# Optimization experiments

Measured on AMD Instinct MI355X. Metric: run time of the kernel, lower is better.

The kernel has to match this reference:

```python
import jax, jax.numpy as jnp
import numpy as np

FEAT_STRIDE = 16
NEG_OV, POS_OV = 0.3, 0.7
RPN_BATCH = 256
NUM_FG = int(0.5 * RPN_BATCH)  # RPN_FG_FRACTION * RPN_BATCHSIZE


def _gen_anchors(base=16, ratios=(0.5, 1.0, 2.0), scales=(4, 8, 16)):
    # 3D extension of the classic generate_anchors: ratio warps w/h, scale multiplies all dims
    ctr = (base - 1) / 2.0
    rows = []
    for r in ratios:
        for s in scales:
            w = base * s * np.sqrt(1.0 / r)
            h = base * s * np.sqrt(r)
            d = float(base * s)
            rows.append([ctr - 0.5 * (w - 1), ctr - 0.5 * (h - 1),
                         ctr + 0.5 * (w - 1), ctr + 0.5 * (h - 1),
                         ctr - 0.5 * (d - 1), ctr + 0.5 * (d - 1)])
    return np.asarray(rows, np.float32)


def setup_inputs() -> dict:
    key = jax.random.key(0)
    ks = jax.random.split(key, 8)
    B, H, W, D, K, A = 2, 48, 48, 24, 20, 9
    cls = jax.random.normal(ks[0], (B, 2 * A, H, W, D), jnp.float32)
    x1 = jax.random.uniform(ks[1], (B, K)) * 600.0
    y1 = jax.random.uniform(ks[2], (B, K)) * 600.0
    z1 = jax.random.uniform(ks[3], (B, K)) * 300.0
    whd = 16.0 + jax.random.uniform(ks[4], (B, K, 3)) * jnp.array([104.0, 104.0, 48.0])
    x2 = jnp.minimum(x1 + whd[..., 0], 767.0)
    y2 = jnp.minimum(y1 + whd[..., 1], 767.0)
    z2 = jnp.minimum(z1 + whd[..., 2], 383.0)
    cid = jax.random.randint(ks[5], (B, K), 1, 4).astype(jnp.float32)
    gt_boxes = jnp.stack([x1, y1, x2, y2, z1, z2, cid], axis=2)
    im_info = jnp.tile(jnp.array([[768.0, 768.0, 384.0]], jnp.float32), (B, 1))
    total = H * W * D * A
    return {
        'rpn_cls_score': cls,
        'gt_boxes': gt_boxes,
        'im_info': im_info,
        'num_boxes': jnp.full((B,), K, jnp.int32),
        'anchors': jnp.asarray(_gen_anchors()),
        'rand_fg': jax.random.uniform(ks[6], (B, total)),
        'rand_bg': jax.random.uniform(ks[7], (B, total)),
    }


def _overlaps(anc, gt):
    # anc: (N,6) [x1,y1,x2,y2,z1,z2]; gt: (B,K,7) -> IoU (B,N,K)
    aw = anc[:, 2] - anc[:, 0] + 1.0
    ah = anc[:, 3] - anc[:, 1] + 1.0
    ad = anc[:, 5] - anc[:, 4] + 1.0
    a_area = aw * ah * ad  # (N,)
    gw = gt[:, :, 2] - gt[:, :, 0] + 1.0
    gh = gt[:, :, 3] - gt[:, :, 1] + 1.0
    gd = gt[:, :, 5] - gt[:, :, 4] + 1.0
    g_area = gw * gh * gd  # (B,K)
    iw = jnp.clip(jnp.minimum(anc[None, :, None, 2], gt[:, None, :, 2]) -
                  jnp.maximum(anc[None, :, None, 0], gt[:, None, :, 0]) + 1.0, 0.0)
    ih = jnp.clip(jnp.minimum(anc[None, :, None, 3], gt[:, None, :, 3]) -
                  jnp.maximum(anc[None, :, None, 1], gt[:, None, :, 1]) + 1.0, 0.0)
    idp = jnp.clip(jnp.minimum(anc[None, :, None, 5], gt[:, None, :, 5]) -
                   jnp.maximum(anc[None, :, None, 4], gt[:, None, :, 4]) + 1.0, 0.0)
    inter = iw * ih * idp
    ov = inter / (a_area[None, :, None] + g_area[:, None, :] - inter)
    gt_zero = (gw == 1.0) & (gh == 1.0) & (gd == 1.0)
    a_zero = (aw == 1.0) & (ah == 1.0) & (ad == 1.0)
    ov = jnp.where(gt_zero[:, None, :], 0.0, ov)
    ov = jnp.where(a_zero[None, :, None], -1.0, ov)
    return ov


def _transform(ex, gt):
    # ex: (N,6); gt: (B,N,6) -> (B,N,6) targets (dx,dy,dz,dw,dh,dd)
    ew = ex[:, 2] - ex[:, 0] + 1.0
    eh = ex[:, 3] - ex[:, 1] + 1.0
    ed = ex[:, 5] - ex[:, 4] + 1.0
    ecx = ex[:, 0] + 0.5 * (ew - 1.0)
    ecy = ex[:, 1] + 0.5 * (eh - 1.0)
    ecz = ex[:, 4] + 0.5 * (ed - 1.0)
    gw = gt[:, :, 2] - gt[:, :, 0] + 1.0
    gh = gt[:, :, 3] - gt[:, :, 1] + 1.0
    gd = gt[:, :, 5] - gt[:, :, 4] + 1.0
    gcx = gt[:, :, 0] + 0.5 * (gw - 1.0)
    gcy = gt[:, :, 1] + 0.5 * (gh - 1.0)
    gcz = gt[:, :, 4] + 0.5 * (gd - 1.0)
    return jnp.stack([(gcx - ecx[None]) / ew[None],
                      (gcy - ecy[None]) / eh[None],
                      (gcz - ecz[None]) / ed[None],
                      jnp.log(gw / ew[None]),
                      jnp.log(gh / eh[None]),
                      jnp.log(gd / ed[None])], axis=2)


def _rank(p):
    # rank of each element when sorted by descending priority, per row
    return jnp.argsort(jnp.argsort(-p, axis=1), axis=1)


def reference(rpn_cls_score, gt_boxes, im_info, num_boxes, anchors, rand_fg, rand_bg):
    B = gt_boxes.shape[0]
    H, W, D = rpn_cls_score.shape[2], rpn_cls_score.shape[3], rpn_cls_score.shape[4]
    A = anchors.shape[0]
    sx = jnp.arange(W, dtype=jnp.float32) * FEAT_STRIDE
    sy = jnp.arange(H, dtype=jnp.float32) * FEAT_STRIDE
    sz = jnp.arange(D, dtype=jnp.float32) * FEAT_STRIDE
    mx, my, mz = jnp.meshgrid(sx, sy, sz, indexing='xy')  # (H,W,D) each
    shifts = jnp.stack([mx.ravel(), my.ravel(), mx.ravel(), my.ravel(), mz.ravel(), mz.ravel()], axis=1)
    all_anchors = (anchors[None, :, :] + shifts[:, None, :]).reshape(-1, 6)  # (total,6)
    total = all_anchors.shape[0]
    inside = ((all_anchors[:, 0] >= 0) & (all_anchors[:, 1] >= 0) & (all_anchors[:, 4] >= 0) &
              (all_anchors[:, 2] < im_info[0, 1]) & (all_anchors[:, 3] < im_info[0, 0]) &
              (all_anchors[:, 5] < im_info[0, 2]))  # (total,)

    ov = _overlaps(all_anchors, gt_boxes)                       # (B,total,K)
    ov_m = jnp.where(inside[None, :, None], ov, -1.0)           # mask outside anchors
    max_ov = ov_m.max(axis=2)
    argmax_ov = jnp.argmax(ov_m, axis=2)                        # (B,total)

    labels = jnp.full((B, total), -1.0, jnp.float32)
    ins = inside[None, :]
    labels = jnp.where(ins & (max_ov < NEG_OV), 0.0, labels)
    gt_max = ov_m.max(axis=1)                                   # (B,K)
    gt_max = jnp.where(gt_max == 0.0, 1e-5, gt_max)
    tie = jnp.sum(ov_m == gt_max[:, None, :], axis=2) > 0
    labels = jnp.where(ins & tie, 1.0, labels)
    labels = jnp.where(ins & (max_ov >= POS_OV), 1.0, labels)

    # fg subsampling: randomly keep at most NUM_FG positives per image
    fg = labels == 1.0
    rk = _rank(jnp.where(fg, rand_fg, -1.0))
    labels = jnp.where(fg & (rk >= NUM_FG), -1.0, labels)
    # bg subsampling: keep RPN_BATCH - num_fg negatives per image
    num_bg = RPN_BATCH - jnp.sum(labels == 1.0, axis=1)         # (B,)
    bg = labels == 0.0
    rkb = _rank(jnp.where(bg, rand_bg, -1.0))
    labels = jnp.where(bg & (rkb >= num_bg[:, None]), -1.0, labels)

    assigned = jnp.take_along_axis(gt_boxes, argmax_ov[:, :, None], axis=1)  # (B,total,7)
    bbox_targets = _transform(all_anchors, assigned[:, :, :6])
    bbox_targets = jnp.where(inside[None, :, None], bbox_targets, 0.0)

    in_w = jnp.where(labels == 1.0, 1.0, 0.0)                   # RPN_BBOX_INSIDE_WEIGHTS[0]=1
    # replicate original bug: weights from the LAST image's example count
    num_examples = jnp.sum(labels[-1] >= 0.0).astype(jnp.float32)
    w = 1.0 / num_examples
    out_w = jnp.where(labels == 1.0, w, jnp.where(labels == 0.0, w, 0.0))

    labels_o = labels.reshape(B, H, W, D, A).transpose(0, 4, 1, 2, 3).reshape(B, 1, A * H * D, W)
    bt_o = bbox_targets.reshape(B, H, W, D, A * 6).transpose(0, 4, 1, 2, 3)
    iw_o = jnp.broadcast_to(in_w[:, :, None], (B, total, 6)).reshape(B, H, W, D, 6 * A).transpose(0, 4, 1, 2, 3)
    ow_o = jnp.broadcast_to(out_w[:, :, None], (B, total, 6)).reshape(B, H, W, D, 6 * A).transpose(0, 4, 1, 2, 3)
    return labels_o, bt_o, iw_o, ow_o
```

## Files before the change

### kernel.cpp

```cpp
#include <hip/hip_runtime.h>
#include <math.h>

#define BB 2
#define HH 48
#define WW 48
#define DD 24
#define KK 20
#define AA 9
#define TOTAL (HH*WW*DD*AA)
#define SPAT (HH*WW*DD)
#define OUT0N (BB*TOTAL)
#define CH 54
#define NB 4096
#define CAPB 256
#define FG_QUOTA 128
#define RPN_B 256
#define STRIDE_F 16.0f

#define O_REC    0
#define O_GTMAX  (OUT0N)
#define O_HIST   (O_GTMAX + BB*KK)
#define O_CUT    (O_HIST + 4*NB)
#define O_W      (O_CUT + 16)
#define O_LIST   (O_W + 1)

__device__ __forceinline__ unsigned enc_f(float f){
  unsigned u = __float_as_uint(f);
  return (u & 0x80000000u) ? ~u : (u | 0x80000000u);
}
__device__ __forceinline__ float dec_f(unsigned u){
  return (u & 0x80000000u) ? __uint_as_float(u & 0x7FFFFFFFu) : __uint_as_float(~u);
}
#define ENC_NEG1 0x407FFFFFu

__device__ __forceinline__ float iou_pre(float ax1,float ay1,float ax2,float ay2,
                                         float az1,float az2,float a_area,
                                         const float* g){
  #pragma clang fp contract(off)
  float iw = fminf(ax2,g[2]) - fmaxf(ax1,g[0]) + 1.0f; iw = fmaxf(iw,0.0f);
  float ih = fminf(ay2,g[3]) - fmaxf(ay1,g[1]) + 1.0f; ih = fmaxf(ih,0.0f);
  float id = fminf(az2,g[5]) - fmaxf(az1,g[4]) + 1.0f; id = fmaxf(id,0.0f);
  float inter = iw*ih*id;
  return inter / ((a_area + g[6]) - inter);
}

__device__ __forceinline__ void gt_derive(const float* gt7, float* g8){
  #pragma clang fp contract(off)
  float gw = gt7[2]-gt7[0]+1.0f, gh = gt7[3]-gt7[1]+1.0f, gd = gt7[5]-gt7[4]+1.0f;
  g8[0]=gt7[0]; g8[1]=gt7[1]; g8[2]=gt7[2]; g8[3]=gt7[3];
  g8[4]=gt7[4]; g8[5]=gt7[5]; g8[6]=gw*gh*gd; g8[7]=0.0f;
}

#define GM_SB 27
__global__ void __launch_bounds__(256) k_gtmax(const float* __restrict__ gt,
    const float* __restrict__ anc, const float* __restrict__ imi,
    unsigned* __restrict__ ws){
  __shared__ float s_gd[KK*8];
  __shared__ float s_a6[6];
  __shared__ float s_im[3];
  __shared__ unsigned s_max[KK];
  int tid = threadIdx.x;
  int a = blockIdx.y;
  int b = blockIdx.z;
  if (b == 0 && a == 0 && blockIdx.x < 16){
    int base = blockIdx.x*256 + tid;
    #pragma unroll
    for (int j=0;j<4;j++) ws[O_HIST + j*NB + base] = 0u;
  }
  if (tid < KK) gt_derive(&gt[(b*KK+tid)*7], &s_gd[tid*8]);
  if (tid < 6)  s_a6[tid] = anc[a*6+tid];
  if (tid < 3)  s_im[tid] = imi[tid];
  if (tid < KK) s_max[tid] = ENC_NEG1;
  __syncthreads();
  float rmax[KK];
  #pragma unroll
  for (int k=0;k<KK;k++) rmax[k] = -1.0f;
  int s0 = blockIdx.x*256 + tid;
  for (int j=0; j<8; j++){
    int s = s0 + j*(GM_SB*256);
    int d = s % DD; int s2 = s / DD;
    int w = s2 % WW; int h = s2 / WW;
    float fx = w*STRIDE_F, fy = h*STRIDE_F, fz = d*STRIDE_F;
    float ax1=s_a6[0]+fx, ay1=s_a6[1]+fy, ax2=s_a6[2]+fx;
    float ay2=s_a6[3]+fy, az1=s_a6[4]+fz, az2=s_a6[5]+fz;
    bool inside = (ax1>=0.f)&&(ay1>=0.f)&&(az1>=0.f)&&
                  (ax2<s_im[1])&&(ay2<s_im[0])&&(az2<s_im[2]);
    if (inside){
      #pragma clang fp contract(off)
      float aw = ax2-ax1+1.0f, ah = ay2-ay1+1.0f, ad = az2-az1+1.0f;
      float a_area = aw*ah*ad;
      #pragma unroll
      for (int k=0;k<KK;k++)
        rmax[k] = fmaxf(rmax[k], iou_pre(ax1,ay1,ax2,ay2,az1,az2,a_area,&s_gd[k*8]));
    }
  }
  #pragma unroll
  for (int k=0;k<KK;k++){
    float v = rmax[k];
    for (int off=32; off>0; off>>=1) v = fmaxf(v, __shfl_down(v, off, 64));
    if ((tid & 63) == 0) atomicMax(&s_max[k], enc_f(v));
  }
  __syncthreads();
  if (tid < KK) atomicMax(&ws[O_GTMAX + b*KK + tid], s_max[tid]);
}

__global__ void __launch_bounds__(256) k_label(const float* __restrict__ gt,
    const float* __restrict__ anc, const float* __restrict__ imi,
    const float* __restrict__ rfg, const float* __restrict__ rbg,
    unsigned* __restrict__ ws){
  __shared__ float s_gd[BB*KK*8];
  __shared__ float s_anc[AA*6];
  __shared__ float s_im[3];
  __shared__ float s_gm[BB*KK];
  int tid = threadIdx.x;
  if (tid < BB*KK) gt_derive(&gt[tid*7], &s_gd[tid*8]);
  for (int j=tid; j<AA*6; j+=256) s_anc[j] = anc[j];
  if (tid<3) s_im[tid] = imi[tid];
  if (tid<BB*KK){ float g = dec_f(ws[O_GTMAX+tid]); if (g==0.0f) g = 1e-5f; s_gm[tid]=g; }
  __syncthreads();
  int t = blockIdx.x*256 + tid;
  int d = t % DD; int r1 = t/DD;
  int w = r1 % WW; int r2 = r1/WW;
  int h = r2 % HH; int r3 = r2/HH;
  int a = r3 % AA; int b = r3/AA;
  int i = ((h*WW+w)*DD + d)*AA + a;
  float fx=w*STRIDE_F, fy=h*STRIDE_F, fz=d*STRIDE_F;
  float ax1=s_anc[a*6+0]+fx, ay1=s_anc[a*6+1]+fy, ax2=s_anc[a*6+2]+fx;
  float ay2=s_anc[a*6+3]+fy, az1=s_anc[a*6+4]+fz, az2=s_anc[a*6+5]+fz;
  bool inside = (ax1>=0.f)&&(ay1>=0.f)&&(az1>=0.f)&&
                (ax2<s_im[1])&&(ay2<s_im[0])&&(az2<s_im[2]);
  float L = -1.0f;
  int am = 0;
  if (inside){
    #pragma clang fp contract(off)
    float aw = ax2-ax1+1.0f, ah = ay2-ay1+1.0f, ad = az2-az1+1.0f;
    float a_area = aw*ah*ad;
    float mv = -2.0f; bool tie = false;
    #pragma unroll
    for (int k=0;k<KK;k++){
      float ov = iou_pre(ax1,ay1,ax2,ay2,az1,az2,a_area,&s_gd[(b*KK+k)*8]);
      if (ov > mv){ mv = ov; am = k; }
      tie = tie || (ov == s_gm[b*KK+k]);
    }
    if (mv < 0.3f) L = 0.0f;
    if (tie)       L = 1.0f;
    if (mv >= 0.7f) L = 1.0f;
  }
  unsigned code = (L==1.0f) ? 2u : ((L==0.0f) ? 1u : 0u);
  unsigned bucket = 0;
  if (code){
    int fl = (code==1u ? 2 : 0) + b;
    const float* ra = (code==1u) ? rbg : rfg;
    float r = ra[b*TOTAL + i];
    bucket = (unsigned)min(NB-1, (int)(r*(float)NB));
    unsigned pos = atomicAdd(&ws[O_HIST + fl*NB + bucket], 1u);
    if (pos < CAPB) ((int*)ws)[O_LIST + ((fl*NB + (int)bucket)<<8) + pos] = i;
  }
  ws[O_REC + t] = code | ((unsigned)am<<2) | (bucket<<7);
}

__global__ void __launch_bounds__(256) k_cuts(unsigned* __restrict__ ws){
  int fl = blockIdx.x; int tid = threadIdx.x;
  int b = fl & 1; int isbg = fl >> 1;
  const int CHK = NB/256;
  __shared__ unsigned ps[256];
  __shared__ unsigned s_fg;
  if (tid == 0) s_fg = 0u;
  __syncthreads();
  unsigned part = 0;
  int hi = NB - CHK*tid;
  for (int j = hi-CHK; j < hi; j++) part += ws[O_HIST + fl*NB + j];
  if (isbg){
    unsigned pf = 0;
    for (int j = tid*CHK; j < (tid+1)*CHK; j++) pf += ws[O_HIST + b*NB + j];
    atomicAdd(&s_fg, pf);
  }
  ps[tid] = part;
  __syncthreads();
  for (int off=1; off<256; off<<=1){
    unsigned v = (tid>=off) ? ps[tid-off] : 0u;
    __syncthreads();
    ps[tid] += v;
    __syncthreads();
  }
  unsigned N = ps[255];
  unsigned excl = ps[tid] - part;
  unsigned F = isbg ? s_fg : N;
  int quota = isbg ? (RPN_B - (int)min(F, (unsigned)FG_QUOTA)) : FG_QUOTA;
  if (fl == 3 && tid == 0){
    int fgk = min((int)F, FG_QUOTA);
    int bgk = min((int)N, RPN_B - fgk);
    ((float*)ws)[O_W] = 1.0f / (float)(fgk + bgk);
  }
  int* cut = (int*)&ws[O_CUT + fl*4];
  if ((int)N <= quota){
    if (tid==0){ cut[0] = -1; cut[1] = 0; cut[2] = quota; cut[3] = 0; }
    return;
  }
  unsigned cum = excl;
  for (int bk = hi-1; bk >= hi-CHK; bk--){
    unsigned c = ws[O_HIST + fl*NB + bk];
    if (c > 0u && (unsigned)(quota-1) >= cum && (unsigned)(quota-1) < cum + c){
      cut[0] = bk; cut[1] = (int)cum; cut[2] = quota; cut[3] = (int)c;
    }
    cum += c;
  }
}

__global__ void __launch_bounds__(256) k_out(const float* __restrict__ gt,
    const float* __restrict__ anc, const float* __restrict__ imi,
    const float* __restrict__ rfg, const float* __restrict__ rbg,
    float* __restrict__ out, const unsigned* __restrict__ ws){
  __shared__ float s_gt[BB*KK*7];
  __shared__ float s_anc[AA*6];
  __shared__ float s_im[3];
  __shared__ float s_w;
  int tid = threadIdx.x;
  for (int j=tid; j<BB*KK*7; j+=256) s_gt[j] = gt[j];
  for (int j=tid; j<AA*6; j+=256) s_anc[j] = anc[j];
  if (tid<3) s_im[tid] = imi[tid];
  if (tid==0) s_w = ((const float*)ws)[O_W];
  __syncthreads();
  int t = blockIdx.x*256 + tid;
  int d = t % DD; int r1=t/DD; int w=r1%WW; int r2=r1/WW;
  int h = r2 % HH; int r3=r2/HH; int a=r3%AA; int b=r3/AA;
  unsigned rec = ws[O_REC + t];
  unsigned code = rec & 3u;
  int am = (int)((rec>>2) & 31u);
  int bucket = (int)((rec>>7) & 4095u);
  float L = (code==2u) ? 1.0f : ((code==1u) ? 0.0f : -1.0f);
  if (code){
    int isbg = (code==1u);
    int fl = isbg*2 + b;
    const int* cut = (const int*)&ws[O_CUT + fl*4];
    int cutb = cut[0];
    if (cutb >= 0){
      if (bucket < cutb) L = -1.0f;
      else if (bucket == cutb){
        int rank_base = cut[1], quota = cut[2];
        int n = min(cut[3], CAPB);
        int i = ((h*WW+w)*DD + d)*AA + a;
        const float* ra = isbg ? rbg : rfg;
        float ri = ra[b*TOTAL + i];
        const int* lst = (const int*)ws + O_LIST + ((fl*NB + cutb)<<8);
        int cnt = 0;
        for (int e=0; e<n; e++){
          int j = lst[e];
          float rj = ra[b*TOTAL + j];
          cnt += (rj > ri) || (rj == ri && j < i);
        }
        if (rank_base + cnt >= quota) L = -1.0f;
      }
    }
  }
  float fx=w*STRIDE_F, fy=h*STRIDE_F, fz=d*STRIDE_F;
  float ax1=s_anc[a*6+0]+fx, ay1=s_anc[a*6+1]+fy, ax2=s_anc[a*6+2]+fx;
  float ay2=s_anc[a*6+3]+fy, az1=s_anc[a*6+4]+fz, az2=s_anc[a*6+5]+fz;
  bool inside = (ax1>=0.f)&&(ay1>=0.f)&&(az1>=0.f)&&
                (ax2<s_im[1])&&(ay2<s_im[0])&&(az2<s_im[2]);
  float bt[6] = {0.f,0.f,0.f,0.f,0.f,0.f};
  if (inside){
    const float* g = &s_gt[(b*KK + am)*7];
    float ew=ax2-ax1+1.f, eh=ay2-ay1+1.f, ed=az2-az1+1.f;
    float ecx=ax1+0.5f*(ew-1.f), ecy=ay1+0.5f*(eh-1.f), ecz=az1+0.5f*(ed-1.f);
    float gw=g[2]-g[0]+1.f, gh=g[3]-g[1]+1.f, gd=g[5]-g[4]+1.f;
    float gcx=g[0]+0.5f*(gw-1.f), gcy=g[1]+0.5f*(gh-1.f), gcz=g[4]+0.5f*(gd-1.f);
    bt[0]=(gcx-ecx)/ew; bt[1]=(gcy-ecy)/eh; bt[2]=(gcz-ecz)/ed;
    bt[3]=logf(gw/ew);  bt[4]=logf(gh/eh);  bt[5]=logf(gd/ed);
  }
  out[t] = L;
  float iwv = (L==1.0f) ? 1.0f : 0.0f;
  float owv = (L==1.0f || L==0.0f) ? s_w : 0.0f;
  int sp = (h*WW + w)*DD + d;
  float* out1 = out + OUT0N;
  float* out2 = out1 + BB*CH*SPAT;
  float* out3 = out2 + BB*CH*SPAT;
  int basech = (b*CH + a*6)*SPAT + sp;
  #pragma unroll
  for (int c=0; c<6; c++){
    int off = basech + c*SPAT;
    out1[off] = bt[c];
    out2[off] = iwv;
    out3[off] = owv;
  }
}

extern "C" void kernel_launch(void* const* d_in, const int* in_sizes, int n_in,
                              void* d_out, int out_size, void* d_ws, size_t ws_size,
                              hipStream_t stream) {
  (void)in_sizes; (void)n_in; (void)out_size; (void)ws_size;
  const float* gt  = (const float*)d_in[1];
  const float* imi = (const float*)d_in[2];
  const float* anc = (const float*)d_in[4];
  const float* rfg = (const float*)d_in[5];
  const float* rbg = (const float*)d_in[6];
  float* out = (float*)d_out;
  unsigned* ws = (unsigned*)d_ws;
  int nb = (OUT0N + 255)/256;
  hipMemsetAsync((char*)d_ws + (size_t)O_GTMAX*4, 0, BB*KK*4, stream);
  k_gtmax <<<dim3(GM_SB, AA, BB), dim3(256), 0, stream>>>(gt, anc, imi, ws);
  k_label <<<dim3(nb), dim3(256), 0, stream>>>(gt, anc, imi, rfg, rbg, ws);
  k_cuts  <<<dim3(4), dim3(256), 0, stream>>>(ws);
  k_out   <<<dim3(nb), dim3(256), 0, stream>>>(gt, anc, imi, rfg, rbg, out, ws);
}
```

Measured before the change: 183.9 us.

## Vectorize output stores, widen gtmax grid, prefetch randoms, and register-cache histogram

The output kernel now has each thread handle four consecutive depth positions, storing labels and the three 54-channel target/weight tensors with float4 writes, and launches a quarter as many blocks. The gtmax kernel gets four times as many blocks with fewer serial iterations each. The label kernel loads both random values before the shared-memory setup barrier so the loads overlap it, and the cuts kernel keeps histogram chunks in registers instead of reading global memory twice. IoU also returns early when the intersection is zero, skipping the divide. These changes target store bandwidth, load latency and occupancy, at the cost of more registers per thread in the output kernel.

```diff
diff --git a/kernel.cpp b/kernel.cpp
--- a/kernel.cpp
+++ b/kernel.cpp
@@ -41,6 +41,7 @@
   float ih = fminf(ay2,g[3]) - fmaxf(ay1,g[1]) + 1.0f; ih = fmaxf(ih,0.0f);
   float id = fminf(az2,g[5]) - fmaxf(az1,g[4]) + 1.0f; id = fmaxf(id,0.0f);
   float inter = iw*ih*id;
+  if (inter <= 0.0f) return 0.0f;
   return inter / ((a_area + g[6]) - inter);
 }
 
@@ -51,7 +52,7 @@
   g8[4]=gt7[4]; g8[5]=gt7[5]; g8[6]=gw*gh*gd; g8[7]=0.0f;
 }
 
-#define GM_SB 27
+#define GM_SB 108
 __global__ void __launch_bounds__(256) k_gtmax(const float* __restrict__ gt,
     const float* __restrict__ anc, const float* __restrict__ imi,
     unsigned* __restrict__ ws){
@@ -76,7 +77,8 @@
   #pragma unroll
   for (int k=0;k<KK;k++) rmax[k] = -1.0f;
   int s0 = blockIdx.x*256 + tid;
-  for (int j=0; j<8; j++){
+  #pragma unroll
+  for (int j=0; j<2; j++){
     int s = s0 + j*(GM_SB*256);
     int d = s % DD; int s2 = s / DD;
     int w = s2 % WW; int h = s2 / WW;
@@ -113,17 +115,19 @@
   __shared__ float s_im[3];
   __shared__ float s_gm[BB*KK];
   int tid = threadIdx.x;
-  if (tid < BB*KK) gt_derive(&gt[tid*7], &s_gd[tid*8]);
-  for (int j=tid; j<AA*6; j+=256) s_anc[j] = anc[j];
-  if (tid<3) s_im[tid] = imi[tid];
-  if (tid<BB*KK){ float g = dec_f(ws[O_GTMAX+tid]); if (g==0.0f) g = 1e-5f; s_gm[tid]=g; }
-  __syncthreads();
   int t = blockIdx.x*256 + tid;
   int d = t % DD; int r1 = t/DD;
   int w = r1 % WW; int r2 = r1/WW;
   int h = r2 % HH; int r3 = r2/HH;
   int a = r3 % AA; int b = r3/AA;
   int i = ((h*WW+w)*DD + d)*AA + a;
+  float rf = rfg[b*TOTAL + i];
+  float rb = rbg[b*TOTAL + i];
+  if (tid < BB*KK) gt_derive(&gt[tid*7], &s_gd[tid*8]);
+  for (int j=tid; j<AA*6; j+=256) s_anc[j] = anc[j];
+  if (tid<3) s_im[tid] = imi[tid];
+  if (tid<BB*KK){ float g = dec_f(ws[O_GTMAX+tid]); if (g==0.0f) g = 1e-5f; s_gm[tid]=g; }
+  __syncthreads();
   float fx=w*STRIDE_F, fy=h*STRIDE_F, fz=d*STRIDE_F;
   float ax1=s_anc[a*6+0]+fx, ay1=s_anc[a*6+1]+fy, ax2=s_anc[a*6+2]+fx;
   float ay2=s_anc[a*6+3]+fy, az1=s_anc[a*6+4]+fz, az2=s_anc[a*6+5]+fz;
@@ -150,8 +154,7 @@
   unsigned bucket = 0;
   if (code){
     int fl = (code==1u ? 2 : 0) + b;
-    const float* ra = (code==1u) ? rbg : rfg;
-    float r = ra[b*TOTAL + i];
+    float r = (code==1u) ? rb : rf;
     bucket = (unsigned)min(NB-1, (int)(r*(float)NB));
     unsigned pos = atomicAdd(&ws[O_HIST + fl*NB + bucket], 1u);
     if (pos < CAPB) ((int*)ws)[O_LIST + ((fl*NB + (int)bucket)<<8) + pos] = i;
@@ -167,12 +170,20 @@
   __shared__ unsigned s_fg;
   if (tid == 0) s_fg = 0u;
   __syncthreads();
+  int hi = NB - CHK*tid;
+  unsigned hv[CHK];
+  #pragma unroll
+  for (int e=0; e<CHK; e++) hv[e] = ws[O_HIST + fl*NB + (hi-CHK+e)];
   unsigned part = 0;
-  int hi = NB - CHK*tid;
-  for (int j = hi-CHK; j < hi; j++) part += ws[O_HIST + fl*NB + j];
+  #pragma unroll
+  for (int e=0; e<CHK; e++) part += hv[e];
   if (isbg){
+    unsigned fv[CHK];
+    #pragma unroll
+    for (int e=0; e<CHK; e++) fv[e] = ws[O_HIST + b*NB + tid*CHK + e];
     unsigned pf = 0;
-    for (int j = tid*CHK; j < (tid+1)*CHK; j++) pf += ws[O_HIST + b*NB + j];
+    #pragma unroll
+    for (int e=0; e<CHK; e++) pf += fv[e];
     atomicAdd(&s_fg, pf);
   }
   ps[tid] = part;
@@ -198,8 +209,10 @@
     return;
   }
   unsigned cum = excl;
-  for (int bk = hi-1; bk >= hi-CHK; bk--){
-    unsigned c = ws[O_HIST + fl*NB + bk];
+  #pragma unroll
+  for (int e=CHK-1; e>=0; e--){
+    int bk = hi-CHK+e;
+    unsigned c = hv[e];
     if (c > 0u && (unsigned)(quota-1) >= cum && (unsigned)(quota-1) < cum + c){
       cut[0] = bk; cut[1] = (int)cum; cut[2] = quota; cut[3] = (int)c;
     }
@@ -221,67 +234,84 @@
   if (tid<3) s_im[tid] = imi[tid];
   if (tid==0) s_w = ((const float*)ws)[O_W];
   __syncthreads();
-  int t = blockIdx.x*256 + tid;
-  int d = t % DD; int r1=t/DD; int w=r1%WW; int r2=r1/WW;
-  int h = r2 % HH; int r3=r2/HH; int a=r3%AA; int b=r3/AA;
-  unsigned rec = ws[O_REC + t];
-  unsigned code = rec & 3u;
-  int am = (int)((rec>>2) & 31u);
-  int bucket = (int)((rec>>7) & 4095u);
-  float L = (code==2u) ? 1.0f : ((code==1u) ? 0.0f : -1.0f);
-  if (code){
-    int isbg = (code==1u);
-    int fl = isbg*2 + b;
-    const int* cut = (const int*)&ws[O_CUT + fl*4];
-    int cutb = cut[0];
-    if (cutb >= 0){
-      if (bucket < cutb) L = -1.0f;
-      else if (bucket == cutb){
-        int rank_base = cut[1], quota = cut[2];
-        int n = min(cut[3], CAPB);
-        int i = ((h*WW+w)*DD + d)*AA + a;
-        const float* ra = isbg ? rbg : rfg;
-        float ri = ra[b*TOTAL + i];
-        const int* lst = (const int*)ws + O_LIST + ((fl*NB + cutb)<<8);
-        int cnt = 0;
-        for (int e=0; e<n; e++){
-          int j = lst[e];
-          float rj = ra[b*TOTAL + j];
-          cnt += (rj > ri) || (rj == ri && j < i);
+  int t4 = (blockIdx.x*256 + tid)*4;
+  int d0 = t4 % DD; int r1=t4/DD;
+  int w = r1 % WW; int r2 = r1/WW;
+  int h = r2 % HH; int r3 = r2/HH;
+  int a = r3 % AA; int b = r3/AA;
+  const uint4 rec4 = *reinterpret_cast<const uint4*>(&ws[O_REC + t4]);
+  unsigned recs[4] = {rec4.x, rec4.y, rec4.z, rec4.w};
+  float sw = s_w;
+  float fx=w*STRIDE_F, fy=h*STRIDE_F;
+  float ax1=s_anc[a*6+0]+fx, ay1=s_anc[a*6+1]+fy;
+  float ax2=s_anc[a*6+2]+fx, ay2=s_anc[a*6+3]+fy;
+  float L4[4], iw4[4], ow4[4], btv[6][4];
+  #pragma unroll
+  for (int dd=0; dd<4; dd++){
+    int d = d0 + dd;
+    unsigned rec = recs[dd];
+    unsigned code = rec & 3u;
+    int am = (int)((rec>>2) & 31u);
+    int bucket = (int)((rec>>7) & 4095u);
+    float L = (code==2u) ? 1.0f : ((code==1u) ? 0.0f : -1.0f);
+    if (code){
+      int isbg = (code==1u);
+      int fl = isbg*2 + b;
+      const int* cut = (const int*)&ws[O_CUT + fl*4];
+      int cutb = cut[0];
+      if (cutb >= 0){
+        if (bucket < cutb) L = -1.0f;
+        else if (bucket == cutb){
+          int rank_base = cut[1], quota = cut[2];
+          int n = min(cut[3], CAPB);
+          int i = ((h*WW+w)*DD + d)*AA + a;
+          const float* ra = isbg ? rbg : rfg;
+          float ri = ra[b*TOTAL + i];
+          const int* lst = (const int*)ws + O_LIST + ((fl*NB + cutb)<<8);
+          int cnt = 0;
+          for (int e=0; e<n; e++){
+            int jj = lst[e];
+            float rj = ra[b*TOTAL + jj];
+            cnt += (rj > ri) || (rj == ri && jj < i);
+          }
+          if (rank_base + cnt >= quota) L = -1.0f;
         }
-        if (rank_base + cnt >= quota) L = -1.0f;
       }
     }
-  }
-  float fx=w*STRIDE_F, fy=h*STRIDE_F, fz=d*STRIDE_F;
-  float ax1=s_anc[a*6+0]+fx, ay1=s_anc[a*6+1]+fy, ax2=s_anc[a*6+2]+fx;
-  float ay2=s_anc[a*6+3]+fy, az1=s_anc[a*6+4]+fz, az2=s_anc[a*6+5]+fz;
-  bool inside = (ax1>=0.f)&&(ay1>=0.f)&&(az1>=0.f)&&
-                (ax2<s_im[1])&&(ay2<s_im[0])&&(az2<s_im[2]);
-  float bt[6] = {0.f,0.f,0.f,0.f,0.f,0.f};
-  if (inside){
-    const float* g = &s_gt[(b*KK + am)*7];
-    float ew=ax2-ax1+1.f, eh=ay2-ay1+1.f, ed=az2-az1+1.f;
-    float ecx=ax1+0.5f*(ew-1.f), ecy=ay1+0.5f*(eh-1.f), ecz=az1+0.5f*(ed-1.f);
-    float gw=g[2]-g[0]+1.f, gh=g[3]-g[1]+1.f, gd=g[5]-g[4]+1.f;
-    float gcx=g[0]+0.5f*(gw-1.f), gcy=g[1]+0.5f*(gh-1.f), gcz=g[4]+0.5f*(gd-1.f);
-    bt[0]=(gcx-ecx)/ew; bt[1]=(gcy-ecy)/eh; bt[2]=(gcz-ecz)/ed;
-    bt[3]=logf(gw/ew);  bt[4]=logf(gh/eh);  bt[5]=logf(gd/ed);
-  }
-  out[t] = L;
-  float iwv = (L==1.0f) ? 1.0f : 0.0f;
-  float owv = (L==1.0f || L==0.0f) ? s_w : 0.0f;
-  int sp = (h*WW + w)*DD + d;
+    float fz = d*STRIDE_F;
+    float az1 = s_anc[a*6+4]+fz, az2 = s_anc[a*6+5]+fz;
+    bool inside = (ax1>=0.f)&&(ay1>=0.f)&&(az1>=0.f)&&
+                  (ax2<s_im[1])&&(ay2<s_im[0])&&(az2<s_im[2]);
+    float bt[6] = {0.f,0.f,0.f,0.f,0.f,0.f};
+    if (inside){
+      const float* g = &s_gt[(b*KK + am)*7];
+      float ew=ax2-ax1+1.f, eh=ay2-ay1+1.f, ed=az2-az1+1.f;
+      float ecx=ax1+0.5f*(ew-1.f), ecy=ay1+0.5f*(eh-1.f), ecz=az1+0.5f*(ed-1.f);
+      float gw=g[2]-g[0]+1.f, gh=g[3]-g[1]+1.f, gd=g[5]-g[4]+1.f;
+      float gcx=g[0]+0.5f*(gw-1.f), gcy=g[1]+0.5f*(gh-1.f), gcz=g[4]+0.5f*(gd-1.f);
+      bt[0]=(gcx-ecx)/ew; bt[1]=(gcy-ecy)/eh; bt[2]=(gcz-ecz)/ed;
+      bt[3]=logf(gw/ew);  bt[4]=logf(gh/eh);  bt[5]=logf(gd/ed);
+    }
+    L4[dd] = L;
+    iw4[dd] = (L==1.0f) ? 1.0f : 0.0f;
+    ow4[dd] = (L==1.0f || L==0.0f) ? sw : 0.0f;
+    #pragma unroll
+    for (int c=0; c<6; c++) btv[c][dd] = bt[c];
+  }
+  *reinterpret_cast<float4*>(&out[t4]) = make_float4(L4[0],L4[1],L4[2],L4[3]);
+  int sp = (h*WW + w)*DD + d0;
   float* out1 = out + OUT0N;
   float* out2 = out1 + BB*CH*SPAT;
   float* out3 = out2 + BB*CH*SPAT;
   int basech = (b*CH + a*6)*SPAT + sp;
+  float4 iwv = make_float4(iw4[0],iw4[1],iw4[2],iw4[3]);
+  float4 owv = make_float4(ow4[0],ow4[1],ow4[2],ow4[3]);
   #pragma unroll
   for (int c=0; c<6; c++){
     int off = basech + c*SPAT;
-    out1[off] = bt[c];
-    out2[off] = iwv;
-    out3[off] = owv;
+    *reinterpret_cast<float4*>(&out1[off]) = make_float4(btv[c][0],btv[c][1],btv[c][2],btv[c][3]);
+    *reinterpret_cast<float4*>(&out2[off]) = iwv;
+    *reinterpret_cast<float4*>(&out3[off]) = owv;
   }
 }
 
@@ -297,9 +327,10 @@
   float* out = (float*)d_out;
   unsigned* ws = (unsigned*)d_ws;
   int nb = (OUT0N + 255)/256;
+  int nb4 = (OUT0N + 1023)/1024;
   hipMemsetAsync((char*)d_ws + (size_t)O_GTMAX*4, 0, BB*KK*4, stream);
   k_gtmax <<<dim3(GM_SB, AA, BB), dim3(256), 0, stream>>>(gt, anc, imi, ws);
   k_label <<<dim3(nb), dim3(256), 0, stream>>>(gt, anc, imi, rfg, rbg, ws);
   k_cuts  <<<dim3(4), dim3(256), 0, stream>>>(ws);
-  k_out   <<<dim3(nb), dim3(256), 0, stream>>>(gt, anc, imi, rfg, rbg, out, ws);
-}
+  k_out   <<<dim3(nb4), dim3(256), 0, stream>>>(gt, anc, imi, rfg, rbg, out, ws);
+}
```

Result: slower. 191.2 us (+4.0%).
